# Performance work log

Measured on AMD Instinct MI355X. Metric: run time of the kernel, lower is better.

Reference implementation:

```python
import jax, jax.numpy as jnp
import numpy as np

FEATS = 1024
HEAD = 16
MLP_HIDDEN = 4096
B, N = 8, 1024
EPS = 1e-5


def _layernorm(x, g, b):
    mu = jnp.mean(x, axis=-1, keepdims=True)
    var = jnp.var(x, axis=-1, keepdims=True)
    return (x - mu) * jax.lax.rsqrt(var + EPS) * g + b


def setup_inputs() -> dict:
    key = jax.random.key(0)
    ks = jax.random.split(key, 12)
    s_attn = 1.0 / np.sqrt(FEATS)
    s_mlp1 = 1.0 / np.sqrt(FEATS)
    s_mlp2 = 1.0 / np.sqrt(MLP_HIDDEN)
    return {
        "x": jax.random.normal(ks[0], (B, N, FEATS), dtype=jnp.float32),
        "ln1_g": jnp.ones((FEATS,), jnp.float32),
        "ln1_b": jnp.zeros((FEATS,), jnp.float32),
        "wq": jax.random.normal(ks[1], (FEATS, FEATS), jnp.float32) * s_attn,
        "bq": jnp.zeros((FEATS,), jnp.float32),
        "wk": jax.random.normal(ks[2], (FEATS, FEATS), jnp.float32) * s_attn,
        "bk": jnp.zeros((FEATS,), jnp.float32),
        "wv": jax.random.normal(ks[3], (FEATS, FEATS), jnp.float32) * s_attn,
        "bv": jnp.zeros((FEATS,), jnp.float32),
        "wo": jax.random.normal(ks[4], (FEATS, FEATS), jnp.float32) * s_attn,
        "bo": jnp.zeros((FEATS,), jnp.float32),
        "ln2_g": jnp.ones((FEATS,), jnp.float32),
        "ln2_b": jnp.zeros((FEATS,), jnp.float32),
        "w1": jax.random.normal(ks[5], (FEATS, MLP_HIDDEN), jnp.float32) * s_mlp1,
        "b1": jnp.zeros((MLP_HIDDEN,), jnp.float32),
        "w2": jax.random.normal(ks[6], (MLP_HIDDEN, FEATS), jnp.float32) * s_mlp2,
        "b2": jnp.zeros((FEATS,), jnp.float32),
    }


def reference(x, ln1_g, ln1_b, wq, bq, wk, bk, wv, bv, wo, bo,
              ln2_g, ln2_b, w1, b1, w2, b2):
    b, n, f = x.shape
    d = f // HEAD
    sqrt_d = jnp.asarray(f, x.dtype) ** 0.5  # NOTE: scale by sqrt(feats), as in source

    h = _layernorm(x, ln1_g, ln1_b)
    # [b, n, f] -> [b, head, n, d]
    q = (h @ wq + bq).reshape(b, n, HEAD, d).transpose(0, 2, 1, 3)
    k = (h @ wk + bk).reshape(b, n, HEAD, d).transpose(0, 2, 1, 3)
    v = (h @ wv + bv).reshape(b, n, HEAD, d).transpose(0, 2, 1, 3)

    score = jnp.einsum('bhif,bhjf->bhij', q, k) / sqrt_d
    p = jax.nn.softmax(score, axis=-1)
    attn = jnp.einsum('bhij,bhjf->bihf', p, v).reshape(b, n, f)
    o = attn @ wo + bo
    out = o + x

    h2 = _layernorm(out, ln2_g, ln2_b)
    m = jax.nn.gelu(h2 @ w1 + b1, approximate=False)
    m = jax.nn.gelu(m @ w2 + b2, approximate=False)
    return m + out
```

## Files before the change

kernel.cpp:

```cpp
#include <hip/hip_runtime.h>
#include <cstdint>

typedef __bf16 bf16;
typedef __attribute__((ext_vector_type(8))) __bf16 bf16x8;
typedef __attribute__((ext_vector_type(4))) __bf16 bf16x4;
typedef __attribute__((ext_vector_type(4))) float f32x4;
typedef __attribute__((ext_vector_type(8))) unsigned short u16x8;

#define AS1C(p) ((const __attribute__((address_space(1))) void*)(p))
#define AS3(p)  ((__attribute__((address_space(3))) void*)(p))

__device__ __forceinline__ float gelu_exact(float v) {
    return 0.5f * v * (1.0f + erff(v * 0.7071067811865476f));
}

__global__ __launch_bounds__(256, 1) void wtrans_kernel(
    const float* __restrict__ w, bf16* __restrict__ wt, int K, int N)
{
    __shared__ float tile[64][65];
    const int k0 = blockIdx.y * 64, n0 = blockIdx.x * 64;
    const int tid = threadIdx.x;
    {
        const int kl = tid >> 2, nc = (tid & 3) * 16;
        #pragma unroll
        for (int i = 0; i < 4; ++i) {
            const float4 v = *(const float4*)&w[(size_t)(k0 + kl) * N + n0 + nc + i * 4];
            tile[kl][nc + i * 4 + 0] = v.x;
            tile[kl][nc + i * 4 + 1] = v.y;
            tile[kl][nc + i * 4 + 2] = v.z;
            tile[kl][nc + i * 4 + 3] = v.w;
        }
    }
    __syncthreads();
    {
        const int nl = tid >> 2, kc = (tid & 3) * 16;
        #pragma unroll
        for (int i = 0; i < 4; ++i) {
            bf16x4 o4;
            o4[0] = (bf16)tile[kc + i * 4 + 0][nl];
            o4[1] = (bf16)tile[kc + i * 4 + 1][nl];
            o4[2] = (bf16)tile[kc + i * 4 + 2][nl];
            o4[3] = (bf16)tile[kc + i * 4 + 3][nl];
            *(bf16x4*)&wt[(size_t)(n0 + nl) * K + k0 + kc + i * 4] = o4;
        }
    }
}

__global__ void bias3_kernel(const float* __restrict__ a, const float* __restrict__ b,
                             const float* __restrict__ c, float* __restrict__ o)
{
    const int i = blockIdx.x * 256 + threadIdx.x;
    o[i] = (i < 1024) ? a[i] : (i < 2048 ? b[i - 1024] : c[i - 2048]);
}

__global__ __launch_bounds__(256, 1) void ln_kernel(
    const float* __restrict__ x, const float* __restrict__ gw,
    const float* __restrict__ bw, bf16* __restrict__ out)
{
    const int row = blockIdx.x, tid = threadIdx.x;
    const float4 v = *(const float4*)&x[(size_t)row * 1024 + tid * 4];
    float s = v.x + v.y + v.z + v.w;
    float q = v.x * v.x + v.y * v.y + v.z * v.z + v.w * v.w;
    #pragma unroll
    for (int off = 32; off > 0; off >>= 1) {
        s += __shfl_xor(s, off);
        q += __shfl_xor(q, off);
    }
    __shared__ float red[8];
    if ((tid & 63) == 0) { red[tid >> 6] = s; red[4 + (tid >> 6)] = q; }
    __syncthreads();
    s = red[0] + red[1] + red[2] + red[3];
    q = red[4] + red[5] + red[6] + red[7];
    const float mu = s * (1.f / 1024.f);
    const float rs = rsqrtf(q * (1.f / 1024.f) - mu * mu + 1e-5f);
    const float4 gg = *(const float4*)&gw[tid * 4];
    const float4 bb = *(const float4*)&bw[tid * 4];
    bf16x4 o4;
    o4[0] = (bf16)((v.x - mu) * rs * gg.x + bb.x);
    o4[1] = (bf16)((v.y - mu) * rs * gg.y + bb.y);
    o4[2] = (bf16)((v.z - mu) * rs * gg.z + bb.z);
    o4[3] = (bf16)((v.w - mu) * rs * gg.w + bb.w);
    *(bf16x4*)&out[(size_t)row * 1024 + tid * 4] = o4;
}

template<int BCH>
__device__ __forceinline__ void stage_tile(
    const bf16* __restrict__ A, const bf16* __restrict__ BT, int K,
    int bm, int bn, int k0, char* buf, int wid, int lanep)
{
    const int rsub = lanep >> 3, ksub = (lanep & 7) * 8;
    #pragma unroll
    for (int c = 0; c < 4; ++c) {
        const bf16* src = A + (size_t)(bm + c * 64 + wid * 8 + rsub) * K + k0 + ksub;
        __builtin_amdgcn_global_load_lds(AS1C(src), AS3(buf + (c * 8 + wid) * 1024), 16, 0, 0);
    }
    #pragma unroll
    for (int c = 0; c < BCH; ++c) {
        const bf16* src = BT + (size_t)(bn + c * 64 + wid * 8 + rsub) * K + k0 + ksub;
        __builtin_amdgcn_global_load_lds(AS1C(src), AS3(buf + 32768 + (c * 8 + wid) * 1024), 16, 0, 0);
    }
}

template<int EPI, int BN>
__global__ __launch_bounds__(512, 2) void gemm8p_kernel(
    const bf16* __restrict__ A, const bf16* __restrict__ BT,
    const float* __restrict__ bias, const float* __restrict__ res,
    void* __restrict__ out, int M, int N, int K)
{
    constexpr int PWM = (BN == 256) ? 128 : 64;
    constexpr int PWN = 64;
    constexpr int MF = PWM / 16;
    constexpr int NF = 4;
    constexpr int MFH = MF / 2;
    constexpr int NFH = 2;
    constexpr int BCH = BN / 64;
    constexpr int BUFB = (256 + BN) * 128;
    constexpr int NBUF = (BN == 256) ? 2 : 3;
    extern __shared__ char lds[];

    const int tid = threadIdx.x;
    const int lane = tid & 63, wid = tid >> 6;
    const int wr = (BN == 256) ? (wid >> 2) : (wid >> 1);
    const int wc = (BN == 256) ? (wid & 3) : (wid & 1);
    const int j = lane & 15, g = lane >> 4;
    const int lanep = lane ^ ((lane >> 4) & 2);

    const int nbn = N / BN;
    const int nwg = (M / 256) * nbn;
    const int bid = blockIdx.x;
    const int wg = (bid & 7) * (nwg >> 3) + (bid >> 3);
    const int bm = (wg / nbn) * 256;
    const int bn = (wg % nbn) * BN;

    f32x4 acc[MF][NF] = {};
    const int NT = K >> 6;

    stage_tile<BCH>(A, BT, K, bm, bn, 0, lds, wid, lanep);
    if constexpr (NBUF == 3) {
        stage_tile<BCH>(A, BT, K, bm, bn, 64, lds + BUFB, wid, lanep);
        asm volatile("s_waitcnt vmcnt(6)" ::: "memory");
    } else {
        asm volatile("s_waitcnt vmcnt(0)" ::: "memory");
    }
    __builtin_amdgcn_s_barrier();

    for (int t = 0; t < NT; ++t) {
        char* buf = lds + ((NBUF == 2) ? (t & 1) : (t % 3)) * BUFB;
        #pragma unroll
        for (int qm = 0; qm < 2; ++qm) {
            bf16x8 af[MFH][2];
            #pragma unroll
            for (int mf = 0; mf < MFH; ++mf)
                #pragma unroll
                for (int ks = 0; ks < 2; ++ks) {
                    const int R = wr * PWM + (qm * MFH + mf) * 16 + j;
                    uint32_t lb = (uint32_t)(R * 128 + ks * 64 + g * 16);
                    lb ^= (uint32_t)(R & 4) << 3;
                    af[mf][ks] = *(const bf16x8*)(buf + lb);
                }
            #pragma unroll
            for (int qn = 0; qn < 2; ++qn) {
                bf16x8 bfr[NFH][2];
                #pragma unroll
                for (int nf = 0; nf < NFH; ++nf)
                    #pragma unroll
                    for (int ks = 0; ks < 2; ++ks) {
                        const int R = wc * PWN + (qn * NFH + nf) * 16 + j;
                        uint32_t lb = (uint32_t)(R * 128 + ks * 64 + g * 16);
                        lb ^= (uint32_t)(R & 4) << 3;
                        bfr[nf][ks] = *(const bf16x8*)(buf + 32768 + lb);
                    }
                if (qm == 0 && qn == 0) {
                    if constexpr (NBUF == 2) {
                        if (t + 1 < NT)
                            stage_tile<BCH>(A, BT, K, bm, bn, (t + 1) << 6,
                                            lds + ((t + 1) & 1) * BUFB, wid, lanep);
                    } else {
                        if (t + 2 < NT)
                            stage_tile<BCH>(A, BT, K, bm, bn, (t + 2) << 6,
                                            lds + ((t + 2) % 3) * BUFB, wid, lanep);
                    }
                }
                __builtin_amdgcn_s_barrier();
                asm volatile("s_waitcnt lgkmcnt(0)" ::: "memory");
                __builtin_amdgcn_sched_barrier(0);
                __builtin_amdgcn_s_setprio(1);
                #pragma unroll
                for (int mf = 0; mf < MFH; ++mf)
                    #pragma unroll
                    for (int nf = 0; nf < NFH; ++nf)
                        #pragma unroll
                        for (int ks = 0; ks < 2; ++ks)
                            acc[qm * MFH + mf][qn * NFH + nf] =
                                __builtin_amdgcn_mfma_f32_16x16x32_bf16(
                                    af[mf][ks], bfr[nf][ks],
                                    acc[qm * MFH + mf][qn * NFH + nf], 0, 0, 0);
                __builtin_amdgcn_s_setprio(0);
                if (qm == 1 && qn == 1) {
                    if constexpr (NBUF == 2) {
                        asm volatile("s_waitcnt vmcnt(0)" ::: "memory");
                    } else {
                        if (t + 2 < NT) asm volatile("s_waitcnt vmcnt(6)" ::: "memory");
                        else            asm volatile("s_waitcnt vmcnt(0)" ::: "memory");
                    }
                }
                __builtin_amdgcn_s_barrier();
            }
        }
    }

    const int row0 = bm + wr * PWM;
    const int col0 = bn + wc * PWN;
    #pragma unroll
    for (int nf = 0; nf < NF; ++nf) {
        const int col = col0 + nf * 16 + j;
        const float bs = bias[col];
        #pragma unroll
        for (int mf = 0; mf < MF; ++mf) {
            #pragma unroll
            for (int r = 0; r < 4; ++r) {
                const int row = row0 + mf * 16 + g * 4 + r;
                float v = acc[mf][nf][r] + bs;
                if constexpr (EPI == 2 || EPI == 3) v = gelu_exact(v);
                if constexpr (EPI == 1 || EPI == 3) {
                    v += res[(size_t)row * N + col];
                    ((float*)out)[(size_t)row * N + col] = v;
                } else {
                    ((bf16*)out)[(size_t)row * N + col] = (bf16)v;
                }
            }
        }
    }
}

__global__ __launch_bounds__(256, 1) void attn_kernel(
    const bf16* __restrict__ qkv, bf16* __restrict__ attn)
{
    const int tid = threadIdx.x;
    const int lane = tid & 63, wid = tid >> 6;
    const int j = lane & 15, g = lane >> 4;

    const int lin = blockIdx.x + blockIdx.y * 16;
    const int virt = (lin & 7) * 256 + (lin >> 3);
    const int bh = virt >> 4, qt = virt & 15;
    const int b = bh >> 4, h = bh & 15;
    const int q0 = qt * 64 + wid * 16;

    const bf16* Qp = qkv + (size_t)b * 1024 * 3072 + h * 64;
    const bf16* Kp = Qp + 1024;
    const bf16* Vp = Qp + 2048;

    __shared__ __attribute__((aligned(16))) uint32_t vTu[2][64][36];

    const int kp = (tid & 31) * 2;
    const int d0 = (tid >> 5) * 8;
    {
        const u16x8 r0 = *(const u16x8*)&Vp[(size_t)kp * 3072 + d0];
        const u16x8 r1 = *(const u16x8*)&Vp[(size_t)(kp + 1) * 3072 + d0];
        #pragma unroll
        for (int i = 0; i < 8; ++i)
            vTu[0][d0 + i][tid & 31] = (uint32_t)r0[i] | ((uint32_t)r1[i] << 16);
    }

    bf16x8 qf0 = *(const bf16x8*)&Qp[(size_t)(q0 + j) * 3072 + g * 8];
    bf16x8 qf1 = *(const bf16x8*)&Qp[(size_t)(q0 + j) * 3072 + 32 + g * 8];
    #pragma unroll
    for (int e = 0; e < 8; ++e) {
        qf0[e] = (bf16)((float)qf0[e] * 0.03125f);
        qf1[e] = (bf16)((float)qf1[e] * 0.03125f);
    }

    const int jperm = (j >> 2) * 8 + (j & 3);

    f32x4 o[4] = {};
    float mrun = -1e30f, lsum = 0.f;
    const f32x4 zero = {0.f, 0.f, 0.f, 0.f};

    __syncthreads();

    for (int c = 0; c < 16; ++c) {
        const int key0 = c * 64;
        u16x8 r0, r1;
        if (c + 1 < 16) {
            const size_t vb = (size_t)(key0 + 64 + kp) * 3072 + d0;
            r0 = *(const u16x8*)&Vp[vb];
            r1 = *(const u16x8*)&Vp[vb + 3072];
        }

        f32x4 s[4];
        #pragma unroll
        for (int t = 0; t < 4; ++t) {
            const int key = key0 + (t >> 1) * 32 + jperm + (t & 1) * 4;
            const bf16x8 kf0 = *(const bf16x8*)&Kp[(size_t)key * 3072 + g * 8];
            const bf16x8 kf1 = *(const bf16x8*)&Kp[(size_t)key * 3072 + 32 + g * 8];
            s[t] = __builtin_amdgcn_mfma_f32_16x16x32_bf16(kf0, qf0, zero, 0, 0, 0);
            s[t] = __builtin_amdgcn_mfma_f32_16x16x32_bf16(kf1, qf1, s[t], 0, 0, 0);
        }

        float cur = fmaxf(fmaxf(s[0][0], s[0][1]), fmaxf(s[0][2], s[0][3]));
        #pragma unroll
        for (int t = 1; t < 4; ++t)
            cur = fmaxf(cur, fmaxf(fmaxf(s[t][0], s[t][1]), fmaxf(s[t][2], s[t][3])));
        cur = fmaxf(cur, __shfl_xor(cur, 16));
        cur = fmaxf(cur, __shfl_xor(cur, 32));

        if (!__all(cur - mrun <= 8.0f)) {
            const float mnew = fmaxf(mrun, cur);
            const float alpha = __expf(mrun - mnew);
            float al[4];
            #pragma unroll
            for (int r = 0; r < 4; ++r) al[r] = __shfl(alpha, g * 4 + r);
            #pragma unroll
            for (int dt = 0; dt < 4; ++dt)
                #pragma unroll
                for (int r = 0; r < 4; ++r) o[dt][r] *= al[r];
            lsum *= alpha;
            mrun = mnew;
        }
        float ps = 0.f;
        #pragma unroll
        for (int t = 0; t < 4; ++t)
            #pragma unroll
            for (int r = 0; r < 4; ++r) {
                const float p = __expf(s[t][r] - mrun);
                s[t][r] = p;
                ps += p;
            }
        lsum += ps;

        bf16x8 pa0, pa1;
        #pragma unroll
        for (int r = 0; r < 4; ++r) {
            pa0[r]     = (bf16)s[0][r];
            pa0[4 + r] = (bf16)s[1][r];
            pa1[r]     = (bf16)s[2][r];
            pa1[4 + r] = (bf16)s[3][r];
        }

        if (c + 1 < 16) {
            #pragma unroll
            for (int i = 0; i < 8; ++i)
                vTu[(c + 1) & 1][d0 + i][tid & 31] = (uint32_t)r0[i] | ((uint32_t)r1[i] << 16);
        }

        #pragma unroll
        for (int dt = 0; dt < 4; ++dt) {
            const bf16* vrow = (const bf16*)&vTu[c & 1][dt * 16 + j][0];
            const bf16x8 vb0 = *(const bf16x8*)(vrow + g * 8);
            const bf16x8 vb1 = *(const bf16x8*)(vrow + 32 + g * 8);
            o[dt] = __builtin_amdgcn_mfma_f32_16x16x32_bf16(pa0, vb0, o[dt], 0, 0, 0);
            o[dt] = __builtin_amdgcn_mfma_f32_16x16x32_bf16(pa1, vb1, o[dt], 0, 0, 0);
        }
        __syncthreads();
    }

    lsum += __shfl_xor(lsum, 16);
    lsum += __shfl_xor(lsum, 32);
    float inv[4];
    #pragma unroll
    for (int r = 0; r < 4; ++r) inv[r] = 1.0f / __shfl(lsum, g * 4 + r);
    #pragma unroll
    for (int dt = 0; dt < 4; ++dt)
        #pragma unroll
        for (int r = 0; r < 4; ++r)
            attn[(size_t)(b * 1024 + q0 + g * 4 + r) * 1024 + h * 64 + dt * 16 + j] =
                (bf16)(o[dt][r] * inv[r]);
}

extern "C" void kernel_launch(void* const* d_in, const int* in_sizes, int n_in,
                              void* d_out, int out_size, void* d_ws, size_t ws_size,
                              hipStream_t stream)
{
    const float* x    = (const float*)d_in[0];
    const float* ln1g = (const float*)d_in[1];
    const float* ln1b = (const float*)d_in[2];
    const float* wq   = (const float*)d_in[3];
    const float* bq   = (const float*)d_in[4];
    const float* wk   = (const float*)d_in[5];
    const float* bk   = (const float*)d_in[6];
    const float* wv   = (const float*)d_in[7];
    const float* bv   = (const float*)d_in[8];
    const float* wo   = (const float*)d_in[9];
    const float* bo   = (const float*)d_in[10];
    const float* ln2g = (const float*)d_in[11];
    const float* ln2b = (const float*)d_in[12];
    const float* w1   = (const float*)d_in[13];
    const float* b1   = (const float*)d_in[14];
    const float* w2   = (const float*)d_in[15];
    const float* b2   = (const float*)d_in[16];

    char* ws = (char*)d_ws;
    bf16* wqkvT = (bf16*)ws;  ws += (size_t)3072 * 1024 * 2;
    bf16* woT   = (bf16*)ws;  ws += (size_t)1024 * 1024 * 2;
    bf16* w1T   = (bf16*)ws;  ws += (size_t)4096 * 1024 * 2;
    bf16* w2T   = (bf16*)ws;  ws += (size_t)1024 * 4096 * 2;
    float* bqkv = (float*)ws; ws += (size_t)3072 * 4;
    bf16* h     = (bf16*)ws;  ws += (size_t)8192 * 1024 * 2;
    bf16* qkv   = (bf16*)ws;  ws += (size_t)8192 * 3072 * 2;
    bf16* attn  = (bf16*)ws;  ws += (size_t)8192 * 1024 * 2;
    float* outf = (float*)ws; ws += (size_t)8192 * 1024 * 4;
    bf16* m1    = (bf16*)ws;  ws += (size_t)8192 * 4096 * 2;

    (void)hipFuncSetAttribute((const void*)gemm8p_kernel<0, 128>,
                              hipFuncAttributeMaxDynamicSharedMemorySize, 147456);
    (void)hipFuncSetAttribute((const void*)gemm8p_kernel<1, 128>,
                              hipFuncAttributeMaxDynamicSharedMemorySize, 147456);
    (void)hipFuncSetAttribute((const void*)gemm8p_kernel<2, 256>,
                              hipFuncAttributeMaxDynamicSharedMemorySize, 131072);
    (void)hipFuncSetAttribute((const void*)gemm8p_kernel<3, 128>,
                              hipFuncAttributeMaxDynamicSharedMemorySize, 147456);

    wtrans_kernel<<<dim3(16, 16), 256, 0, stream>>>(wq, wqkvT,                   1024, 1024);
    wtrans_kernel<<<dim3(16, 16), 256, 0, stream>>>(wk, wqkvT + 1024 * 1024,     1024, 1024);
    wtrans_kernel<<<dim3(16, 16), 256, 0, stream>>>(wv, wqkvT + 2 * 1024 * 1024, 1024, 1024);
    wtrans_kernel<<<dim3(16, 16), 256, 0, stream>>>(wo, woT, 1024, 1024);
    wtrans_kernel<<<dim3(64, 16), 256, 0, stream>>>(w1, w1T, 1024, 4096);
    wtrans_kernel<<<dim3(16, 64), 256, 0, stream>>>(w2, w2T, 4096, 1024);
    bias3_kernel<<<12, 256, 0, stream>>>(bq, bk, bv, bqkv);

    ln_kernel<<<8192, 256, 0, stream>>>(x, ln1g, ln1b, h);
    gemm8p_kernel<0, 128><<<768, 512, 147456, stream>>>(h, wqkvT, bqkv, nullptr, qkv, 8192, 3072, 1024);
    attn_kernel<<<dim3(16, 128), 256, 0, stream>>>(qkv, attn);
    gemm8p_kernel<1, 128><<<256, 512, 147456, stream>>>(attn, woT, bo, x, outf, 8192, 1024, 1024);
    ln_kernel<<<8192, 256, 0, stream>>>(outf, ln2g, ln2b, h);
    gemm8p_kernel<2, 256><<<512, 512, 131072, stream>>>(h, w1T, b1, nullptr, m1, 8192, 4096, 1024);
    gemm8p_kernel<3, 128><<<256, 512, 147456, stream>>>(m1, w2T, b2, outf, (float*)d_out, 8192, 1024, 4096);
}
```

Before: 559.6 us.

## Retile GEMM LDS phases, widen swizzle, and prefetch K fragments in attention

```diff
diff --git a/kernel.cpp b/kernel.cpp
--- a/kernel.cpp
+++ b/kernel.cpp
@@ -86,9 +86,8 @@
 template<int BCH>
 __device__ __forceinline__ void stage_tile(
     const bf16* __restrict__ A, const bf16* __restrict__ BT, int K,
-    int bm, int bn, int k0, char* buf, int wid, int lanep)
-{
-    const int rsub = lanep >> 3, ksub = (lanep & 7) * 8;
+    int bm, int bn, int k0, char* buf, int wid, int rsub, int ksub)
+{
     #pragma unroll
     for (int c = 0; c < 4; ++c) {
         const bf16* src = A + (size_t)(bm + c * 64 + wid * 8 + rsub) * K + k0 + ksub;
@@ -111,8 +110,10 @@
     constexpr int PWN = 64;
     constexpr int MF = PWM / 16;
     constexpr int NF = 4;
-    constexpr int MFH = MF / 2;
-    constexpr int NFH = 2;
+    constexpr int PH_M = (BN == 256) ? 4 : 2;
+    constexpr int PH_N = (BN == 256) ? 2 : 4;
+    constexpr int QN = NF / PH_N;
+    constexpr int NPH = (MF / PH_M) * QN;
     constexpr int BCH = BN / 64;
     constexpr int BUFB = (256 + BN) * 128;
     constexpr int NBUF = (BN == 256) ? 2 : 3;
@@ -123,7 +124,8 @@
     const int wr = (BN == 256) ? (wid >> 2) : (wid >> 1);
     const int wc = (BN == 256) ? (wid & 3) : (wid & 1);
     const int j = lane & 15, g = lane >> 4;
-    const int lanep = lane ^ ((lane >> 4) & 2);
+    const int lanep = (lane & 7) ^ ((lane >> 4) & 3) ^ ((wid & 1) << 2);
+    const int rsub = lane >> 3, ksub = lanep * 8;
 
     const int nbn = N / BN;
     const int nwg = (M / 256) * nbn;
@@ -135,9 +137,9 @@
     f32x4 acc[MF][NF] = {};
     const int NT = K >> 6;
 
-    stage_tile<BCH>(A, BT, K, bm, bn, 0, lds, wid, lanep);
+    stage_tile<BCH>(A, BT, K, bm, bn, 0, lds, wid, rsub, ksub);
     if constexpr (NBUF == 3) {
-        stage_tile<BCH>(A, BT, K, bm, bn, 64, lds + BUFB, wid, lanep);
+        stage_tile<BCH>(A, BT, K, bm, bn, 64, lds + BUFB, wid, rsub, ksub);
         asm volatile("s_waitcnt vmcnt(6)" ::: "memory");
     } else {
         asm volatile("s_waitcnt vmcnt(0)" ::: "memory");
@@ -147,65 +149,62 @@
     for (int t = 0; t < NT; ++t) {
         char* buf = lds + ((NBUF == 2) ? (t & 1) : (t % 3)) * BUFB;
         #pragma unroll
-        for (int qm = 0; qm < 2; ++qm) {
-            bf16x8 af[MFH][2];
+        for (int ph = 0; ph < NPH; ++ph) {
+            const int qm = ph / QN, qn = ph % QN;
+            bf16x8 af[PH_M][2], bfr[PH_N][2];
             #pragma unroll
-            for (int mf = 0; mf < MFH; ++mf)
+            for (int mf = 0; mf < PH_M; ++mf)
                 #pragma unroll
                 for (int ks = 0; ks < 2; ++ks) {
-                    const int R = wr * PWM + (qm * MFH + mf) * 16 + j;
+                    const int R = wr * PWM + (qm * PH_M + mf) * 16 + j;
                     uint32_t lb = (uint32_t)(R * 128 + ks * 64 + g * 16);
-                    lb ^= (uint32_t)(R & 4) << 3;
+                    lb ^= (lb >> 4) & 0x70u;
                     af[mf][ks] = *(const bf16x8*)(buf + lb);
                 }
             #pragma unroll
-            for (int qn = 0; qn < 2; ++qn) {
-                bf16x8 bfr[NFH][2];
+            for (int nf = 0; nf < PH_N; ++nf)
                 #pragma unroll
-                for (int nf = 0; nf < NFH; ++nf)
+                for (int ks = 0; ks < 2; ++ks) {
+                    const int R = wc * PWN + (qn * PH_N + nf) * 16 + j;
+                    uint32_t lb = (uint32_t)(R * 128 + ks * 64 + g * 16);
+                    lb ^= (lb >> 4) & 0x70u;
+                    bfr[nf][ks] = *(const bf16x8*)(buf + 32768 + lb);
+                }
+            if (ph == 0) {
+                if constexpr (NBUF == 2) {
+                    if (t + 1 < NT)
+                        stage_tile<BCH>(A, BT, K, bm, bn, (t + 1) << 6,
+                                        lds + ((t + 1) & 1) * BUFB, wid, rsub, ksub);
+                } else {
+                    if (t + 2 < NT)
+                        stage_tile<BCH>(A, BT, K, bm, bn, (t + 2) << 6,
+                                        lds + ((t + 2) % 3) * BUFB, wid, rsub, ksub);
+                }
+            }
+            __builtin_amdgcn_s_barrier();
+            asm volatile("s_waitcnt lgkmcnt(0)" ::: "memory");
+            __builtin_amdgcn_sched_barrier(0);
+            __builtin_amdgcn_s_setprio(1);
+            #pragma unroll
+            for (int mf = 0; mf < PH_M; ++mf)
+                #pragma unroll
+                for (int nf = 0; nf < PH_N; ++nf)
                     #pragma unroll
-                    for (int ks = 0; ks < 2; ++ks) {
-                        const int R = wc * PWN + (qn * NFH + nf) * 16 + j;
-                        uint32_t lb = (uint32_t)(R * 128 + ks * 64 + g * 16);
-                        lb ^= (uint32_t)(R & 4) << 3;
-                        bfr[nf][ks] = *(const bf16x8*)(buf + 32768 + lb);
-                    }
-                if (qm == 0 && qn == 0) {
-                    if constexpr (NBUF == 2) {
-                        if (t + 1 < NT)
-                            stage_tile<BCH>(A, BT, K, bm, bn, (t + 1) << 6,
-                                            lds + ((t + 1) & 1) * BUFB, wid, lanep);
-                    } else {
-                        if (t + 2 < NT)
-                            stage_tile<BCH>(A, BT, K, bm, bn, (t + 2) << 6,
-                                            lds + ((t + 2) % 3) * BUFB, wid, lanep);
-                    }
+                    for (int ks = 0; ks < 2; ++ks)
+                        acc[qm * PH_M + mf][qn * PH_N + nf] =
+                            __builtin_amdgcn_mfma_f32_16x16x32_bf16(
+                                af[mf][ks], bfr[nf][ks],
+                                acc[qm * PH_M + mf][qn * PH_N + nf], 0, 0, 0);
+            __builtin_amdgcn_s_setprio(0);
+            if (ph == NPH - 1) {
+                if constexpr (NBUF == 2) {
+                    asm volatile("s_waitcnt vmcnt(0)" ::: "memory");
+                } else {
+                    if (t + 2 < NT) asm volatile("s_waitcnt vmcnt(6)" ::: "memory");
+                    else            asm volatile("s_waitcnt vmcnt(0)" ::: "memory");
                 }
-                __builtin_amdgcn_s_barrier();
-                asm volatile("s_waitcnt lgkmcnt(0)" ::: "memory");
-                __builtin_amdgcn_sched_barrier(0);
-                __builtin_amdgcn_s_setprio(1);
-                #pragma unroll
-                for (int mf = 0; mf < MFH; ++mf)
-                    #pragma unroll
-                    for (int nf = 0; nf < NFH; ++nf)
-                        #pragma unroll
-                        for (int ks = 0; ks < 2; ++ks)
-                            acc[qm * MFH + mf][qn * NFH + nf] =
-                                __builtin_amdgcn_mfma_f32_16x16x32_bf16(
-                                    af[mf][ks], bfr[nf][ks],
-                                    acc[qm * MFH + mf][qn * NFH + nf], 0, 0, 0);
-                __builtin_amdgcn_s_setprio(0);
-                if (qm == 1 && qn == 1) {
-                    if constexpr (NBUF == 2) {
-                        asm volatile("s_waitcnt vmcnt(0)" ::: "memory");
-                    } else {
-                        if (t + 2 < NT) asm volatile("s_waitcnt vmcnt(6)" ::: "memory");
-                        else            asm volatile("s_waitcnt vmcnt(0)" ::: "memory");
-                    }
-                }
-                __builtin_amdgcn_s_barrier();
             }
+            __builtin_amdgcn_s_barrier();
         }
     }
 
@@ -233,6 +232,97 @@
     }
 }
 
+__device__ __forceinline__ void attn_iter(
+    int c, const bf16* __restrict__ Kp, const bf16* __restrict__ Vp,
+    uint32_t (&vTu)[2][64][36],
+    bf16x8 (&kf)[4][2], bf16x8 (&kfn)[4][2],
+    const bf16x8& qf0, const bf16x8& qf1,
+    f32x4 (&o)[4], float& mrun, float& lsum,
+    int kp, int d0, int jperm, int g, int j)
+{
+    const f32x4 zero = {0.f, 0.f, 0.f, 0.f};
+    const bool pf = (c + 1 < 16);
+
+    u16x8 r0, r1;
+    if (pf) {
+        const size_t vb = (size_t)((c + 1) * 64 + kp) * 3072 + d0;
+        r0 = *(const u16x8*)&Vp[vb];
+        r1 = *(const u16x8*)&Vp[vb + 3072];
+    }
+
+    f32x4 s[4];
+    #pragma unroll
+    for (int t = 0; t < 4; ++t) {
+        s[t] = __builtin_amdgcn_mfma_f32_16x16x32_bf16(kf[t][0], qf0, zero, 0, 0, 0);
+        s[t] = __builtin_amdgcn_mfma_f32_16x16x32_bf16(kf[t][1], qf1, s[t], 0, 0, 0);
+    }
+
+    if (pf) {
+        #pragma unroll
+        for (int t = 0; t < 4; ++t) {
+            const int key = (c + 1) * 64 + (t >> 1) * 32 + jperm + (t & 1) * 4;
+            kfn[t][0] = *(const bf16x8*)&Kp[(size_t)key * 3072 + g * 8];
+            kfn[t][1] = *(const bf16x8*)&Kp[(size_t)key * 3072 + 32 + g * 8];
+        }
+    }
+
+    float cur = fmaxf(fmaxf(s[0][0], s[0][1]), fmaxf(s[0][2], s[0][3]));
+    #pragma unroll
+    for (int t = 1; t < 4; ++t)
+        cur = fmaxf(cur, fmaxf(fmaxf(s[t][0], s[t][1]), fmaxf(s[t][2], s[t][3])));
+    cur = fmaxf(cur, __shfl_xor(cur, 16));
+    cur = fmaxf(cur, __shfl_xor(cur, 32));
+
+    if (!__all(cur - mrun <= 8.0f)) {
+        const float mnew = fmaxf(mrun, cur);
+        const float alpha = __expf(mrun - mnew);
+        float al[4];
+        #pragma unroll
+        for (int r = 0; r < 4; ++r) al[r] = __shfl(alpha, g * 4 + r);
+        #pragma unroll
+        for (int dt = 0; dt < 4; ++dt)
+            #pragma unroll
+            for (int r = 0; r < 4; ++r) o[dt][r] *= al[r];
+        lsum *= alpha;
+        mrun = mnew;
+    }
+    float ps = 0.f;
+    #pragma unroll
+    for (int t = 0; t < 4; ++t)
+        #pragma unroll
+        for (int r = 0; r < 4; ++r) {
+            const float p = __expf(s[t][r] - mrun);
+            s[t][r] = p;
+            ps += p;
+        }
+    lsum += ps;
+
+    bf16x8 pa0, pa1;
+    #pragma unroll
+    for (int r = 0; r < 4; ++r) {
+        pa0[r]     = (bf16)s[0][r];
+        pa0[4 + r] = (bf16)s[1][r];
+        pa1[r]     = (bf16)s[2][r];
+        pa1[4 + r] = (bf16)s[3][r];
+    }
+
+    if (pf) {
+        #pragma unroll
+        for (int i = 0; i < 8; ++i)
+            vTu[(c + 1) & 1][d0 + i][kp >> 1] = (uint32_t)r0[i] | ((uint32_t)r1[i] << 16);
+    }
+
+    #pragma unroll
+    for (int dt = 0; dt < 4; ++dt) {
+        const bf16* vrow = (const bf16*)&vTu[c & 1][dt * 16 + j][0];
+        const bf16x8 vb0 = *(const bf16x8*)(vrow + g * 8);
+        const bf16x8 vb1 = *(const bf16x8*)(vrow + 32 + g * 8);
+        o[dt] = __builtin_amdgcn_mfma_f32_16x16x32_bf16(pa0, vb0, o[dt], 0, 0, 0);
+        o[dt] = __builtin_amdgcn_mfma_f32_16x16x32_bf16(pa1, vb1, o[dt], 0, 0, 0);
+    }
+    __syncthreads();
+}
+
 __global__ __launch_bounds__(256, 1) void attn_kernel(
     const bf16* __restrict__ qkv, bf16* __restrict__ attn)
 {
@@ -259,7 +349,7 @@
         const u16x8 r1 = *(const u16x8*)&Vp[(size_t)(kp + 1) * 3072 + d0];
         #pragma unroll
         for (int i = 0; i < 8; ++i)
-            vTu[0][d0 + i][tid & 31] = (uint32_t)r0[i] | ((uint32_t)r1[i] << 16);
+            vTu[0][d0 + i][kp >> 1] = (uint32_t)r0[i] | ((uint32_t)r1[i] << 16);
     }
 
     bf16x8 qf0 = *(const bf16x8*)&Qp[(size_t)(q0 + j) * 3072 + g * 8];
@@ -274,84 +364,20 @@
 
     f32x4 o[4] = {};
     float mrun = -1e30f, lsum = 0.f;
-    const f32x4 zero = {0.f, 0.f, 0.f, 0.f};
+
+    bf16x8 kfA[4][2], kfB[4][2];
+    #pragma unroll
+    for (int t = 0; t < 4; ++t) {
+        const int key = (t >> 1) * 32 + jperm + (t & 1) * 4;
+        kfA[t][0] = *(const bf16x8*)&Kp[(size_t)key * 3072 + g * 8];
+        kfA[t][1] = *(const bf16x8*)&Kp[(size_t)key * 3072 + 32 + g * 8];
+    }
 
     __syncthreads();
 
-    for (int c = 0; c < 16; ++c) {
-        const int key0 = c * 64;
-        u16x8 r0, r1;
-        if (c + 1 < 16) {
-            const size_t vb = (size_t)(key0 + 64 + kp) * 3072 + d0;
-            r0 = *(const u16x8*)&Vp[vb];
-            r1 = *(const u16x8*)&Vp[vb + 3072];
-        }
-
-        f32x4 s[4];
-        #pragma unroll
-        for (int t = 0; t < 4; ++t) {
-            const int key = key0 + (t >> 1) * 32 + jperm + (t & 1) * 4;
-            const bf16x8 kf0 = *(const bf16x8*)&Kp[(size_t)key * 3072 + g * 8];
-            const bf16x8 kf1 = *(const bf16x8*)&Kp[(size_t)key * 3072 + 32 + g * 8];
-            s[t] = __builtin_amdgcn_mfma_f32_16x16x32_bf16(kf0, qf0, zero, 0, 0, 0);
-            s[t] = __builtin_amdgcn_mfma_f32_16x16x32_bf16(kf1, qf1, s[t], 0, 0, 0);
-        }
-
-        float cur = fmaxf(fmaxf(s[0][0], s[0][1]), fmaxf(s[0][2], s[0][3]));
-        #pragma unroll
-        for (int t = 1; t < 4; ++t)
-            cur = fmaxf(cur, fmaxf(fmaxf(s[t][0], s[t][1]), fmaxf(s[t][2], s[t][3])));
-        cur = fmaxf(cur, __shfl_xor(cur, 16));
-        cur = fmaxf(cur, __shfl_xor(cur, 32));
-
-        if (!__all(cur - mrun <= 8.0f)) {
-            const float mnew = fmaxf(mrun, cur);
-            const float alpha = __expf(mrun - mnew);
-            float al[4];
-            #pragma unroll
-            for (int r = 0; r < 4; ++r) al[r] = __shfl(alpha, g * 4 + r);
-            #pragma unroll
-            for (int dt = 0; dt < 4; ++dt)
-                #pragma unroll
-                for (int r = 0; r < 4; ++r) o[dt][r] *= al[r];
-            lsum *= alpha;
-            mrun = mnew;
-        }
-        float ps = 0.f;
-        #pragma unroll
-        for (int t = 0; t < 4; ++t)
-            #pragma unroll
-            for (int r = 0; r < 4; ++r) {
-                const float p = __expf(s[t][r] - mrun);
-                s[t][r] = p;
-                ps += p;
-            }
-        lsum += ps;
-
-        bf16x8 pa0, pa1;
-        #pragma unroll
-        for (int r = 0; r < 4; ++r) {
-            pa0[r]     = (bf16)s[0][r];
-            pa0[4 + r] = (bf16)s[1][r];
-            pa1[r]     = (bf16)s[2][r];
-            pa1[4 + r] = (bf16)s[3][r];
-        }
-
-        if (c + 1 < 16) {
-            #pragma unroll
-            for (int i = 0; i < 8; ++i)
-                vTu[(c + 1) & 1][d0 + i][tid & 31] = (uint32_t)r0[i] | ((uint32_t)r1[i] << 16);
-        }
-
-        #pragma unroll
-        for (int dt = 0; dt < 4; ++dt) {
-            const bf16* vrow = (const bf16*)&vTu[c & 1][dt * 16 + j][0];
-            const bf16x8 vb0 = *(const bf16x8*)(vrow + g * 8);
-            const bf16x8 vb1 = *(const bf16x8*)(vrow + 32 + g * 8);
-            o[dt] = __builtin_amdgcn_mfma_f32_16x16x32_bf16(pa0, vb0, o[dt], 0, 0, 0);
-            o[dt] = __builtin_amdgcn_mfma_f32_16x16x32_bf16(pa1, vb1, o[dt], 0, 0, 0);
-        }
-        __syncthreads();
+    for (int cc = 0; cc < 16; cc += 2) {
+        attn_iter(cc,     Kp, Vp, vTu, kfA, kfB, qf0, qf1, o, mrun, lsum, kp, d0, jperm, g, j);
+        attn_iter(cc + 1, Kp, Vp, vTu, kfB, kfA, qf0, qf1, o, mrun, lsum, kp, d0, jperm, g, j);
     }
 
     lsum += __shfl_xor(lsum, 16);
```

Result: no change. 553.2 us (-1.2%).
